# Kernel optimization log

Hardware: AMD Instinct MI355X
Metric: run time of the kernel (lower is better)

## Reference

```python
import jax, jax.numpy as jnp
import numpy as np

VOCAB, EMB, H, OUT = 32000, 512, 1024, 32000
SEQ, B = 512, 64

def setup_inputs() -> dict:
    key = jax.random.key(0)
    ks = jax.random.split(key, 16)
    sc = lambda *s: 1.0 / np.sqrt(s[-1])
    return {
        "x": jax.random.randint(ks[0], (B,), 0, VOCAB),
        "encoder_states": jax.random.normal(ks[1], (SEQ, B, 2 * H), jnp.float32),
        "hidden": jax.random.normal(ks[2], (1, B, H), jnp.float32),
        "cell": jax.random.normal(ks[3], (1, B, H), jnp.float32),
        "emb_table": jax.random.normal(ks[4], (VOCAB, EMB), jnp.float32),
        "energy_W": jax.random.normal(ks[5], (1, 3 * H), jnp.float32) * sc(1, 3 * H),
        "energy_b": jnp.zeros((1,), jnp.float32),
        "W_ih": jax.random.normal(ks[6], (4 * H, 2 * H + EMB), jnp.float32) * sc(1, H),
        "W_hh": jax.random.normal(ks[7], (4 * H, H), jnp.float32) * sc(1, H),
        "b_ih": jnp.zeros((4 * H,), jnp.float32),
        "b_hh": jnp.zeros((4 * H,), jnp.float32),
        "fc_W": jax.random.normal(ks[8], (OUT, H), jnp.float32) * sc(1, H),
        "fc_b": jnp.zeros((OUT,), jnp.float32),
    }

def reference(x, encoder_states, hidden, cell, emb_table, energy_W, energy_b,
              W_ih, W_hh, b_ih, b_hh, fc_W, fc_b):
    S = encoder_states.shape[0]
    emb = emb_table[x]                                     # [B, E] (dropout is identity at p=0)
    h_rep = jnp.broadcast_to(hidden, (S,) + hidden.shape[1:])   # [S, B, H]
    cat = jnp.concatenate([h_rep, encoder_states], axis=2)      # [S, B, 3H]
    energy = jax.nn.relu(jnp.einsum('sbk,ok->sbo', cat, energy_W) + energy_b)  # [S, B, 1]
    attn = jax.nn.softmax(energy[..., 0], axis=0)                # softmax over seq dim -> [S, B]
    context = jnp.einsum('sb,sbd->bd', attn, encoder_states)     # [B, 2H]
    rnn_in = jnp.concatenate([context, emb], axis=1)             # [B, 2H+E]
    gates = rnn_in @ W_ih.T + b_ih + hidden[0] @ W_hh.T + b_hh   # [B, 4H]
    i, f, g, o = jnp.split(gates, 4, axis=1)
    i, f, o = jax.nn.sigmoid(i), jax.nn.sigmoid(f), jax.nn.sigmoid(o)
    g = jnp.tanh(g)
    c_new = f * cell[0] + i * g
    h_new = o * jnp.tanh(c_new)
    preds = h_new @ fc_W.T + fc_b                                # [B, OUT]
    return preds, h_new[None], c_new[None]
```

## Files before the change

### kernel.cpp

```cpp
#include <hip/hip_runtime.h>

#define S_LEN 512
#define BATCH 64
#define HDIM  1024
#define TWOH  2048
#define EMB   512
#define KDIM  2560
#define KTOT  3584
#define VOUT  32000

#define WS_MS    64
#define WS_CTX   2112
#define WS_GP    WS_CTX
#define WS_RNNB  (WS_CTX + 64*16*2048)
#define WS_HB16  (WS_RNNB + 114688)

typedef __attribute__((ext_vector_type(8))) short bf16x8;
typedef __attribute__((ext_vector_type(4))) float f32x4;

__device__ __forceinline__ float sigmoidf_(float x) { return 1.f/(1.f+__expf(-x)); }

__device__ __forceinline__ unsigned short f2bf(float f) {
  union { float f; unsigned u; } v; v.f = f;
  return (unsigned short)((v.u + 0x7fffu + ((v.u >> 16) & 1u)) >> 16);
}

__global__ __launch_bounds__(256) void k_attn(const float* __restrict__ enc,
                                              const float* __restrict__ eW,
                                              const float* __restrict__ eb,
                                              const float* __restrict__ hidden,
                                              float* __restrict__ ws_ms,
                                              float* __restrict__ ws_ctx) {
  __shared__ float lds_ms[4][2];
  __shared__ float lds_ctx[4][2048];
  const int lane  = threadIdx.x & 63;
  const int wave  = threadIdx.x >> 6;
  const int chunk = blockIdx.x;
  const int b     = blockIdx.y;

  float hba = 0.f;
  for (int k = lane; k < HDIM; k += 64) hba += hidden[b*HDIM + k] * eW[k];
#pragma unroll
  for (int st = 32; st >= 1; st >>= 1) hba += __shfl_xor(hba, st, 64);
  const float hb = hba + eb[0];

  float4 w4[8];
#pragma unroll
  for (int k = 0; k < 8; ++k)
    w4[k] = *reinterpret_cast<const float4*>(eW + HDIM + 4*lane + 256*k);

  const int s0 = chunk*32 + wave*8;
  const float* base = enc + ((size_t)(s0*BATCH + b))*TWOH + 4*lane;

  float m = 0.f, ssum = 0.f;
  float4 ctx[8];
#pragma unroll
  for (int k = 0; k < 8; ++k) ctx[k] = make_float4(0.f, 0.f, 0.f, 0.f);

  float4 va[8], vb[8];
#pragma unroll
  for (int k = 0; k < 8; ++k) va[k] = *reinterpret_cast<const float4*>(base + 256*k);

#define ATTN_STEP(VCUR, VNXT, I)                                              \
  {                                                                           \
    if ((I) < 7) {                                                            \
      const float* pn = base + (size_t)((I)+1)*BATCH*TWOH;                    \
      _Pragma("unroll")                                                       \
      for (int k = 0; k < 8; ++k)                                             \
        VNXT[k] = *reinterpret_cast<const float4*>(pn + 256*k);               \
    }                                                                         \
    float a = 0.f;                                                            \
    _Pragma("unroll")                                                         \
    for (int k = 0; k < 8; ++k)                                               \
      a += VCUR[k].x*w4[k].x + VCUR[k].y*w4[k].y +                            \
           VCUR[k].z*w4[k].z + VCUR[k].w*w4[k].w;                             \
    _Pragma("unroll")                                                         \
    for (int st = 1; st < 64; st <<= 1) a += __shfl_xor(a, st, 64);           \
    const float e = fmaxf(a + hb, 0.f);                                       \
    if (e > m) {                                                              \
      const float sc = __expf(m - e);                                         \
      ssum = ssum*sc + 1.f;                                                   \
      _Pragma("unroll")                                                       \
      for (int k = 0; k < 8; ++k) {                                           \
        ctx[k].x = fmaf(ctx[k].x, sc, VCUR[k].x);                             \
        ctx[k].y = fmaf(ctx[k].y, sc, VCUR[k].y);                             \
        ctx[k].z = fmaf(ctx[k].z, sc, VCUR[k].z);                             \
        ctx[k].w = fmaf(ctx[k].w, sc, VCUR[k].w);                             \
      }                                                                       \
      m = e;                                                                  \
    } else {                                                                  \
      const float pw = __expf(e - m);                                         \
      ssum += pw;                                                             \
      _Pragma("unroll")                                                       \
      for (int k = 0; k < 8; ++k) {                                           \
        ctx[k].x = fmaf(pw, VCUR[k].x, ctx[k].x);                             \
        ctx[k].y = fmaf(pw, VCUR[k].y, ctx[k].y);                             \
        ctx[k].z = fmaf(pw, VCUR[k].z, ctx[k].z);                             \
        ctx[k].w = fmaf(pw, VCUR[k].w, ctx[k].w);                             \
      }                                                                       \
    }                                                                         \
  }

  ATTN_STEP(va, vb, 0)
  ATTN_STEP(vb, va, 1)
  ATTN_STEP(va, vb, 2)
  ATTN_STEP(vb, va, 3)
  ATTN_STEP(va, vb, 4)
  ATTN_STEP(vb, va, 5)
  ATTN_STEP(va, vb, 6)
  ATTN_STEP(vb, va, 7)
#undef ATTN_STEP

  if (lane == 0) { lds_ms[wave][0] = m; lds_ms[wave][1] = ssum; }
  __syncthreads();
  const float M = fmaxf(fmaxf(lds_ms[0][0], lds_ms[1][0]),
                        fmaxf(lds_ms[2][0], lds_ms[3][0]));
  const float wsc = __expf(m - M);
  float ssum_c = 0.f;
#pragma unroll
  for (int w = 0; w < 4; ++w) ssum_c += __expf(lds_ms[w][0] - M) * lds_ms[w][1];
#pragma unroll
  for (int k = 0; k < 8; ++k) {
    float4 c = ctx[k];
    c.x *= wsc; c.y *= wsc; c.z *= wsc; c.w *= wsc;
    *reinterpret_cast<float4*>(&lds_ctx[wave][4*lane + 256*k]) = c;
  }
  __syncthreads();
  float* outp = ws_ctx + ((size_t)b*16 + chunk)*TWOH;
  for (int d = threadIdx.x; d < TWOH; d += 256)
    outp[d] = lds_ctx[0][d] + lds_ctx[1][d] + lds_ctx[2][d] + lds_ctx[3][d];
  if (threadIdx.x == 0) {
    ws_ms[((size_t)b*16 + chunk)*2]     = M;
    ws_ms[((size_t)b*16 + chunk)*2 + 1] = ssum_c;
  }
}

__global__ __launch_bounds__(256) void k_combine(const float* __restrict__ ws_ms,
                                                 const float* __restrict__ ws_ctx,
                                                 const float* __restrict__ hidden,
                                                 const float* __restrict__ emb_table,
                                                 const int* __restrict__ x,
                                                 unsigned short* __restrict__ rnnB) {
  const int b = blockIdx.x;
  float mc[16], sc[16];
#pragma unroll
  for (int c = 0; c < 16; ++c) {
    mc[c] = ws_ms[(b*16 + c)*2];
    sc[c] = ws_ms[(b*16 + c)*2 + 1];
  }
  float M = mc[0];
#pragma unroll
  for (int c = 1; c < 16; ++c) M = fmaxf(M, mc[c]);
  float wc[16], Ssum = 0.f;
#pragma unroll
  for (int c = 0; c < 16; ++c) { wc[c] = __expf(mc[c] - M); Ssum += wc[c]*sc[c]; }
  const float inv = 1.f / Ssum;
  unsigned short* rb = rnnB + (size_t)b*KTOT;
  for (int d = threadIdx.x; d < TWOH; d += 256) {
    float a = 0.f;
#pragma unroll
    for (int c = 0; c < 16; ++c) a += wc[c] * ws_ctx[((size_t)b*16 + c)*TWOH + d];
    rb[d] = f2bf(a * inv);
  }
  const int xb = x[b];
  for (int e = threadIdx.x; e < EMB; e += 256)
    rb[TWOH + e] = f2bf(emb_table[(size_t)xb*EMB + e]);
  for (int k = threadIdx.x; k < HDIM; k += 256)
    rb[KDIM + k] = f2bf(hidden[b*HDIM + k]);
}

__global__ __launch_bounds__(256) void k_gates(const unsigned short* __restrict__ rnnB,
                                               const float* __restrict__ W_ih,
                                               const float* __restrict__ W_hh,
                                               float* __restrict__ ws_gp) {
  const int lane = threadIdx.x & 63;
  const int wave = threadIdx.x >> 6;
  const int part = blockIdx.x & 7;
  const int rg   = blockIdx.x >> 3;
  const int row0 = rg*64 + wave*16;
  const int mlo  = lane & 15;
  const int kg   = lane >> 4;
  const int j    = row0 + mlo;

  f32x4 acc0 = {0.f,0.f,0.f,0.f}, acc1 = acc0, acc2 = acc0, acc3 = acc0;

  for (int k0 = 0; k0 < 448; k0 += 32) {
    const int kbase = part*448 + k0;
    const float* wsrc = (kbase < KDIM)
        ? (W_ih + (size_t)j*KDIM + kbase + kg*8)
        : (W_hh + (size_t)j*HDIM + (kbase - KDIM) + kg*8);
    const float4 wa = *reinterpret_cast<const float4*>(wsrc);
    const float4 wb = *reinterpret_cast<const float4*>(wsrc + 4);
    bf16x8 afrag;
    afrag[0] = f2bf(wa.x); afrag[1] = f2bf(wa.y);
    afrag[2] = f2bf(wa.z); afrag[3] = f2bf(wa.w);
    afrag[4] = f2bf(wb.x); afrag[5] = f2bf(wb.y);
    afrag[6] = f2bf(wb.z); afrag[7] = f2bf(wb.w);

    const size_t ko = kbase + kg*8;
    const bf16x8 b0 = *reinterpret_cast<const bf16x8*>(rnnB + (size_t)(mlo     )*KTOT + ko);
    const bf16x8 b1 = *reinterpret_cast<const bf16x8*>(rnnB + (size_t)(mlo + 16)*KTOT + ko);
    const bf16x8 b2 = *reinterpret_cast<const bf16x8*>(rnnB + (size_t)(mlo + 32)*KTOT + ko);
    const bf16x8 b3 = *reinterpret_cast<const bf16x8*>(rnnB + (size_t)(mlo + 48)*KTOT + ko);

    acc0 = __builtin_amdgcn_mfma_f32_16x16x32_bf16(afrag, b0, acc0, 0, 0, 0);
    acc1 = __builtin_amdgcn_mfma_f32_16x16x32_bf16(afrag, b1, acc1, 0, 0, 0);
    acc2 = __builtin_amdgcn_mfma_f32_16x16x32_bf16(afrag, b2, acc2, 0, 0, 0);
    acc3 = __builtin_amdgcn_mfma_f32_16x16x32_bf16(afrag, b3, acc3, 0, 0, 0);
  }

  const int mbase = row0 + kg*4;
#define G_ST(ACC, N)                                                          \
  {                                                                           \
    _Pragma("unroll")                                                         \
    for (int jj = 0; jj < 4; ++jj)                                            \
      ws_gp[((size_t)part*4096 + mbase + jj)*64 + ((N)*16 + mlo)] = ACC[jj];  \
  }
  G_ST(acc0, 0) G_ST(acc1, 1) G_ST(acc2, 2) G_ST(acc3, 3)
#undef G_ST
}

__global__ __launch_bounds__(256) void k_lstm(const float* __restrict__ ws_gp,
                                              const float* __restrict__ b_ih,
                                              const float* __restrict__ b_hh,
                                              const float* __restrict__ cell,
                                              float* __restrict__ out_h,
                                              float* __restrict__ out_c,
                                              unsigned short* __restrict__ hB) {
  const int id = blockIdx.x*256 + threadIdx.x;
  const int h = id >> 6, b = id & 63;
  float g[4];
#pragma unroll
  for (int gg = 0; gg < 4; ++gg) {
    const int j = gg*1024 + h;
    float v = b_ih[j] + b_hh[j];
#pragma unroll
    for (int p = 0; p < 8; ++p) v += ws_gp[((size_t)p*4096 + j)*64 + b];
    g[gg] = v;
  }
  const float iv = sigmoidf_(g[0]);
  const float fv = sigmoidf_(g[1]);
  const float gv = tanhf(g[2]);
  const float ov = sigmoidf_(g[3]);
  const float cold = cell[b*HDIM + h];
  const float cn = fmaf(fv, cold, iv*gv);
  const float hn = ov * tanhf(cn);
  out_h[b*HDIM + h] = hn;
  out_c[b*HDIM + h] = cn;
  hB[(size_t)b*HDIM + h] = f2bf(hn);
}

__global__ __launch_bounds__(256) void k_fc(const unsigned short* __restrict__ hB,
                                            const float* __restrict__ fc_W,
                                            const float* __restrict__ fc_b,
                                            float* __restrict__ preds) {
  const int lane = threadIdx.x & 63;
  const int wave = threadIdx.x >> 6;
  const int row0 = (blockIdx.x*4 + wave)*16;
  const int mlo  = lane & 15;
  const int kg   = lane >> 4;

  const float* wrow = fc_W + (size_t)(row0 + mlo)*HDIM + kg*8;

  f32x4 acc0 = {0.f,0.f,0.f,0.f}, acc1 = acc0, acc2 = acc0, acc3 = acc0;

  for (int k0 = 0; k0 < HDIM; k0 += 32) {
    const float4 wa = *reinterpret_cast<const float4*>(wrow + k0);
    const float4 wb = *reinterpret_cast<const float4*>(wrow + k0 + 4);
    bf16x8 afrag;
    afrag[0] = f2bf(wa.x); afrag[1] = f2bf(wa.y);
    afrag[2] = f2bf(wa.z); afrag[3] = f2bf(wa.w);
    afrag[4] = f2bf(wb.x); afrag[5] = f2bf(wb.y);
    afrag[6] = f2bf(wb.z); afrag[7] = f2bf(wb.w);

    const size_t ko = k0 + kg*8;
    const bf16x8 b0 = *reinterpret_cast<const bf16x8*>(hB + (size_t)(mlo     )*HDIM + ko);
    const bf16x8 b1 = *reinterpret_cast<const bf16x8*>(hB + (size_t)(mlo + 16)*HDIM + ko);
    const bf16x8 b2 = *reinterpret_cast<const bf16x8*>(hB + (size_t)(mlo + 32)*HDIM + ko);
    const bf16x8 b3 = *reinterpret_cast<const bf16x8*>(hB + (size_t)(mlo + 48)*HDIM + ko);

    acc0 = __builtin_amdgcn_mfma_f32_16x16x32_bf16(afrag, b0, acc0, 0, 0, 0);
    acc1 = __builtin_amdgcn_mfma_f32_16x16x32_bf16(afrag, b1, acc1, 0, 0, 0);
    acc2 = __builtin_amdgcn_mfma_f32_16x16x32_bf16(afrag, b2, acc2, 0, 0, 0);
    acc3 = __builtin_amdgcn_mfma_f32_16x16x32_bf16(afrag, b3, acc3, 0, 0, 0);
  }

  const int mbase = row0 + kg*4;
  const float4 bias = make_float4(fc_b[mbase], fc_b[mbase+1],
                                  fc_b[mbase+2], fc_b[mbase+3]);
#define FC_STORE(ACC, N)                                                      \
  {                                                                           \
    float4 st = make_float4(ACC[0] + bias.x, ACC[1] + bias.y,                 \
                            ACC[2] + bias.z, ACC[3] + bias.w);                \
    *reinterpret_cast<float4*>(preds + (size_t)((N)*16 + mlo)*VOUT + mbase) = st; \
  }
  FC_STORE(acc0, 0) FC_STORE(acc1, 1) FC_STORE(acc2, 2) FC_STORE(acc3, 3)
#undef FC_STORE
}

extern "C" void kernel_launch(void* const* d_in, const int* in_sizes, int n_in,
                              void* d_out, int out_size, void* d_ws, size_t ws_size,
                              hipStream_t stream) {
  const int*   x      = (const int*)  d_in[0];
  const float* enc    = (const float*)d_in[1];
  const float* hidden = (const float*)d_in[2];
  const float* cell   = (const float*)d_in[3];
  const float* embt   = (const float*)d_in[4];
  const float* eW     = (const float*)d_in[5];
  const float* eb     = (const float*)d_in[6];
  const float* W_ih   = (const float*)d_in[7];
  const float* W_hh   = (const float*)d_in[8];
  const float* b_ih   = (const float*)d_in[9];
  const float* b_hh   = (const float*)d_in[10];
  const float* fc_W   = (const float*)d_in[11];
  const float* fc_b   = (const float*)d_in[12];

  float* out   = (float*)d_out;
  float* preds = out;
  float* out_h = out + (size_t)BATCH*VOUT;
  float* out_c = out_h + BATCH*HDIM;
  float* ws    = (float*)d_ws;
  unsigned short* rnnB = (unsigned short*)(ws + WS_RNNB);
  unsigned short* hB   = (unsigned short*)(ws + WS_HB16);

  k_attn<<<dim3(16, 64), 256, 0, stream>>>(enc, eW, eb, hidden, ws + WS_MS, ws + WS_CTX);
  k_combine<<<64, 256, 0, stream>>>(ws + WS_MS, ws + WS_CTX, hidden, embt, x, rnnB);
  k_gates<<<512, 256, 0, stream>>>(rnnB, W_ih, W_hh, ws + WS_GP);
  k_lstm<<<256, 256, 0, stream>>>(ws + WS_GP, b_ih, b_hh, cell, out_h, out_c, hB);
  k_fc<<<500, 256, 0, stream>>>(hB, fc_W, fc_b, preds);
}
```

Before: 150.5 us.

## Software-pipeline GEMV weight loads in gates/fc and widen combine grid

Both MFMA kernels (gates and fc) now fully unroll the K loop and double-buffer register fragments. The next 64-wide K slice of weights and activations is loaded while the current slice is converted to bf16 and fed to MFMA, which puts more memory requests in flight to hide global-load latency on the weight stream. The combine kernel now uses a 14x64 grid with one element per thread instead of 64 blocks looping. Register pressure rises from the doubled fragment buffers, and each combine thread recomputes the softmax chunk weights redundantly.

```diff
diff --git a/kernel.cpp b/kernel.cpp
--- a/kernel.cpp
+++ b/kernel.cpp
@@ -23,6 +23,15 @@
 __device__ __forceinline__ unsigned short f2bf(float f) {
   union { float f; unsigned u; } v; v.f = f;
   return (unsigned short)((v.u + 0x7fffu + ((v.u >> 16) & 1u)) >> 16);
+}
+
+__device__ __forceinline__ bf16x8 cvt_frag(const float4& a, const float4& b) {
+  bf16x8 r;
+  r[0] = (short)f2bf(a.x); r[1] = (short)f2bf(a.y);
+  r[2] = (short)f2bf(a.z); r[3] = (short)f2bf(a.w);
+  r[4] = (short)f2bf(b.x); r[5] = (short)f2bf(b.y);
+  r[6] = (short)f2bf(b.z); r[7] = (short)f2bf(b.w);
+  return r;
 }
 
 __global__ __launch_bounds__(256) void k_attn(const float* __restrict__ enc,
@@ -141,32 +150,34 @@
                                                  const float* __restrict__ emb_table,
                                                  const int* __restrict__ x,
                                                  unsigned short* __restrict__ rnnB) {
-  const int b = blockIdx.x;
-  float mc[16], sc[16];
-#pragma unroll
-  for (int c = 0; c < 16; ++c) {
-    mc[c] = ws_ms[(b*16 + c)*2];
-    sc[c] = ws_ms[(b*16 + c)*2 + 1];
-  }
-  float M = mc[0];
-#pragma unroll
-  for (int c = 1; c < 16; ++c) M = fmaxf(M, mc[c]);
-  float wc[16], Ssum = 0.f;
-#pragma unroll
-  for (int c = 0; c < 16; ++c) { wc[c] = __expf(mc[c] - M); Ssum += wc[c]*sc[c]; }
-  const float inv = 1.f / Ssum;
+  const int b = blockIdx.y;
+  const int k = blockIdx.x*256 + threadIdx.x;
   unsigned short* rb = rnnB + (size_t)b*KTOT;
-  for (int d = threadIdx.x; d < TWOH; d += 256) {
+
+  if (k < TWOH) {
+    float mc[16], sc[16];
+#pragma unroll
+    for (int c = 0; c < 16; ++c) {
+      mc[c] = ws_ms[(b*16 + c)*2];
+      sc[c] = ws_ms[(b*16 + c)*2 + 1];
+    }
+    float M = mc[0];
+#pragma unroll
+    for (int c = 1; c < 16; ++c) M = fmaxf(M, mc[c]);
+    float wc[16], Ssum = 0.f;
+#pragma unroll
+    for (int c = 0; c < 16; ++c) { wc[c] = __expf(mc[c] - M); Ssum += wc[c]*sc[c]; }
+    const float inv = 1.f / Ssum;
     float a = 0.f;
 #pragma unroll
-    for (int c = 0; c < 16; ++c) a += wc[c] * ws_ctx[((size_t)b*16 + c)*TWOH + d];
-    rb[d] = f2bf(a * inv);
-  }
-  const int xb = x[b];
-  for (int e = threadIdx.x; e < EMB; e += 256)
-    rb[TWOH + e] = f2bf(emb_table[(size_t)xb*EMB + e]);
-  for (int k = threadIdx.x; k < HDIM; k += 256)
-    rb[KDIM + k] = f2bf(hidden[b*HDIM + k]);
+    for (int c = 0; c < 16; ++c) a += wc[c] * ws_ctx[((size_t)b*16 + c)*TWOH + k];
+    rb[k] = f2bf(a * inv);
+  } else if (k < KDIM) {
+    const int xb = x[b];
+    rb[k] = f2bf(emb_table[(size_t)xb*EMB + (k - TWOH)]);
+  } else {
+    rb[k] = f2bf(hidden[b*HDIM + (k - KDIM)]);
+  }
 }
 
 __global__ __launch_bounds__(256) void k_gates(const unsigned short* __restrict__ rnnB,
@@ -181,33 +192,61 @@
   const int mlo  = lane & 15;
   const int kg   = lane >> 4;
   const int j    = row0 + mlo;
+  const unsigned short* rp0 = rnnB + (size_t)mlo*KTOT;
 
   f32x4 acc0 = {0.f,0.f,0.f,0.f}, acc1 = acc0, acc2 = acc0, acc3 = acc0;
 
-  for (int k0 = 0; k0 < 448; k0 += 32) {
-    const int kbase = part*448 + k0;
-    const float* wsrc = (kbase < KDIM)
-        ? (W_ih + (size_t)j*KDIM + kbase + kg*8)
-        : (W_hh + (size_t)j*HDIM + (kbase - KDIM) + kg*8);
-    const float4 wa = *reinterpret_cast<const float4*>(wsrc);
-    const float4 wb = *reinterpret_cast<const float4*>(wsrc + 4);
-    bf16x8 afrag;
-    afrag[0] = f2bf(wa.x); afrag[1] = f2bf(wa.y);
-    afrag[2] = f2bf(wa.z); afrag[3] = f2bf(wa.w);
-    afrag[4] = f2bf(wb.x); afrag[5] = f2bf(wb.y);
-    afrag[6] = f2bf(wb.z); afrag[7] = f2bf(wb.w);
-
-    const size_t ko = kbase + kg*8;
-    const bf16x8 b0 = *reinterpret_cast<const bf16x8*>(rnnB + (size_t)(mlo     )*KTOT + ko);
-    const bf16x8 b1 = *reinterpret_cast<const bf16x8*>(rnnB + (size_t)(mlo + 16)*KTOT + ko);
-    const bf16x8 b2 = *reinterpret_cast<const bf16x8*>(rnnB + (size_t)(mlo + 32)*KTOT + ko);
-    const bf16x8 b3 = *reinterpret_cast<const bf16x8*>(rnnB + (size_t)(mlo + 48)*KTOT + ko);
-
-    acc0 = __builtin_amdgcn_mfma_f32_16x16x32_bf16(afrag, b0, acc0, 0, 0, 0);
-    acc1 = __builtin_amdgcn_mfma_f32_16x16x32_bf16(afrag, b1, acc1, 0, 0, 0);
-    acc2 = __builtin_amdgcn_mfma_f32_16x16x32_bf16(afrag, b2, acc2, 0, 0, 0);
-    acc3 = __builtin_amdgcn_mfma_f32_16x16x32_bf16(afrag, b3, acc3, 0, 0, 0);
-  }
+  float4  Aa[4], Ab[4];
+  bf16x8  Ba[8], Bb[8];
+
+#define G_LOAD(AW, BB, S)                                                     \
+  {                                                                           \
+    const int kb0 = part*448 + (S)*64;                                        \
+    const int kb1 = kb0 + 32;                                                 \
+    const float* ws0 = (kb0 < KDIM) ? (W_ih + (size_t)j*KDIM + kb0 + kg*8)    \
+                                    : (W_hh + (size_t)j*HDIM + (kb0-KDIM) + kg*8); \
+    const float* ws1 = (kb1 < KDIM) ? (W_ih + (size_t)j*KDIM + kb1 + kg*8)    \
+                                    : (W_hh + (size_t)j*HDIM + (kb1-KDIM) + kg*8); \
+    AW[0] = *reinterpret_cast<const float4*>(ws0);                            \
+    AW[1] = *reinterpret_cast<const float4*>(ws0 + 4);                        \
+    AW[2] = *reinterpret_cast<const float4*>(ws1);                            \
+    AW[3] = *reinterpret_cast<const float4*>(ws1 + 4);                        \
+    const size_t ko0 = (size_t)kb0 + kg*8;                                    \
+    const size_t ko1 = (size_t)kb1 + kg*8;                                    \
+    BB[0] = *reinterpret_cast<const bf16x8*>(rp0 + ko0);                      \
+    BB[1] = *reinterpret_cast<const bf16x8*>(rp0 + 16*KTOT + ko0);            \
+    BB[2] = *reinterpret_cast<const bf16x8*>(rp0 + 32*KTOT + ko0);            \
+    BB[3] = *reinterpret_cast<const bf16x8*>(rp0 + 48*KTOT + ko0);            \
+    BB[4] = *reinterpret_cast<const bf16x8*>(rp0 + ko1);                      \
+    BB[5] = *reinterpret_cast<const bf16x8*>(rp0 + 16*KTOT + ko1);            \
+    BB[6] = *reinterpret_cast<const bf16x8*>(rp0 + 32*KTOT + ko1);            \
+    BB[7] = *reinterpret_cast<const bf16x8*>(rp0 + 48*KTOT + ko1);            \
+  }
+
+#define G_COMP(AW, BB)                                                        \
+  {                                                                           \
+    const bf16x8 af0 = cvt_frag(AW[0], AW[1]);                                \
+    const bf16x8 af1 = cvt_frag(AW[2], AW[3]);                                \
+    acc0 = __builtin_amdgcn_mfma_f32_16x16x32_bf16(af0, BB[0], acc0, 0, 0, 0);\
+    acc1 = __builtin_amdgcn_mfma_f32_16x16x32_bf16(af0, BB[1], acc1, 0, 0, 0);\
+    acc2 = __builtin_amdgcn_mfma_f32_16x16x32_bf16(af0, BB[2], acc2, 0, 0, 0);\
+    acc3 = __builtin_amdgcn_mfma_f32_16x16x32_bf16(af0, BB[3], acc3, 0, 0, 0);\
+    acc0 = __builtin_amdgcn_mfma_f32_16x16x32_bf16(af1, BB[4], acc0, 0, 0, 0);\
+    acc1 = __builtin_amdgcn_mfma_f32_16x16x32_bf16(af1, BB[5], acc1, 0, 0, 0);\
+    acc2 = __builtin_amdgcn_mfma_f32_16x16x32_bf16(af1, BB[6], acc2, 0, 0, 0);\
+    acc3 = __builtin_amdgcn_mfma_f32_16x16x32_bf16(af1, BB[7], acc3, 0, 0, 0);\
+  }
+
+  G_LOAD(Aa, Ba, 0)
+  G_LOAD(Ab, Bb, 1) G_COMP(Aa, Ba)
+  G_LOAD(Aa, Ba, 2) G_COMP(Ab, Bb)
+  G_LOAD(Ab, Bb, 3) G_COMP(Aa, Ba)
+  G_LOAD(Aa, Ba, 4) G_COMP(Ab, Bb)
+  G_LOAD(Ab, Bb, 5) G_COMP(Aa, Ba)
+  G_LOAD(Aa, Ba, 6) G_COMP(Ab, Bb)
+  G_COMP(Aa, Ba)
+#undef G_LOAD
+#undef G_COMP
 
   const int mbase = row0 + kg*4;
 #define G_ST(ACC, N)                                                          \
@@ -261,29 +300,62 @@
   const int kg   = lane >> 4;
 
   const float* wrow = fc_W + (size_t)(row0 + mlo)*HDIM + kg*8;
+  const unsigned short* hp = hB + (size_t)mlo*HDIM + kg*8;
 
   f32x4 acc0 = {0.f,0.f,0.f,0.f}, acc1 = acc0, acc2 = acc0, acc3 = acc0;
 
-  for (int k0 = 0; k0 < HDIM; k0 += 32) {
-    const float4 wa = *reinterpret_cast<const float4*>(wrow + k0);
-    const float4 wb = *reinterpret_cast<const float4*>(wrow + k0 + 4);
-    bf16x8 afrag;
-    afrag[0] = f2bf(wa.x); afrag[1] = f2bf(wa.y);
-    afrag[2] = f2bf(wa.z); afrag[3] = f2bf(wa.w);
-    afrag[4] = f2bf(wb.x); afrag[5] = f2bf(wb.y);
-    afrag[6] = f2bf(wb.z); afrag[7] = f2bf(wb.w);
-
-    const size_t ko = k0 + kg*8;
-    const bf16x8 b0 = *reinterpret_cast<const bf16x8*>(hB + (size_t)(mlo     )*HDIM + ko);
-    const bf16x8 b1 = *reinterpret_cast<const bf16x8*>(hB + (size_t)(mlo + 16)*HDIM + ko);
-    const bf16x8 b2 = *reinterpret_cast<const bf16x8*>(hB + (size_t)(mlo + 32)*HDIM + ko);
-    const bf16x8 b3 = *reinterpret_cast<const bf16x8*>(hB + (size_t)(mlo + 48)*HDIM + ko);
-
-    acc0 = __builtin_amdgcn_mfma_f32_16x16x32_bf16(afrag, b0, acc0, 0, 0, 0);
-    acc1 = __builtin_amdgcn_mfma_f32_16x16x32_bf16(afrag, b1, acc1, 0, 0, 0);
-    acc2 = __builtin_amdgcn_mfma_f32_16x16x32_bf16(afrag, b2, acc2, 0, 0, 0);
-    acc3 = __builtin_amdgcn_mfma_f32_16x16x32_bf16(afrag, b3, acc3, 0, 0, 0);
-  }
+  float4  Aa[4], Ab[4];
+  bf16x8  Ba[8], Bb[8];
+
+#define FC_LOAD(AW, BB, K0)                                                   \
+  {                                                                           \
+    AW[0] = *reinterpret_cast<const float4*>(wrow + (K0));                    \
+    AW[1] = *reinterpret_cast<const float4*>(wrow + (K0) + 4);                \
+    AW[2] = *reinterpret_cast<const float4*>(wrow + (K0) + 32);               \
+    AW[3] = *reinterpret_cast<const float4*>(wrow + (K0) + 36);               \
+    BB[0] = *reinterpret_cast<const bf16x8*>(hp + (K0));                      \
+    BB[1] = *reinterpret_cast<const bf16x8*>(hp + 16*HDIM + (K0));            \
+    BB[2] = *reinterpret_cast<const bf16x8*>(hp + 32*HDIM + (K0));            \
+    BB[3] = *reinterpret_cast<const bf16x8*>(hp + 48*HDIM + (K0));            \
+    BB[4] = *reinterpret_cast<const bf16x8*>(hp + (K0) + 32);                 \
+    BB[5] = *reinterpret_cast<const bf16x8*>(hp + 16*HDIM + (K0) + 32);       \
+    BB[6] = *reinterpret_cast<const bf16x8*>(hp + 32*HDIM + (K0) + 32);       \
+    BB[7] = *reinterpret_cast<const bf16x8*>(hp + 48*HDIM + (K0) + 32);       \
+  }
+
+#define FC_COMP(AW, BB)                                                       \
+  {                                                                           \
+    const bf16x8 af0 = cvt_frag(AW[0], AW[1]);                                \
+    const bf16x8 af1 = cvt_frag(AW[2], AW[3]);                                \
+    acc0 = __builtin_amdgcn_mfma_f32_16x16x32_bf16(af0, BB[0], acc0, 0, 0, 0);\
+    acc1 = __builtin_amdgcn_mfma_f32_16x16x32_bf16(af0, BB[1], acc1, 0, 0, 0);\
+    acc2 = __builtin_amdgcn_mfma_f32_16x16x32_bf16(af0, BB[2], acc2, 0, 0, 0);\
+    acc3 = __builtin_amdgcn_mfma_f32_16x16x32_bf16(af0, BB[3], acc3, 0, 0, 0);\
+    acc0 = __builtin_amdgcn_mfma_f32_16x16x32_bf16(af1, BB[4], acc0, 0, 0, 0);\
+    acc1 = __builtin_amdgcn_mfma_f32_16x16x32_bf16(af1, BB[5], acc1, 0, 0, 0);\
+    acc2 = __builtin_amdgcn_mfma_f32_16x16x32_bf16(af1, BB[6], acc2, 0, 0, 0);\
+    acc3 = __builtin_amdgcn_mfma_f32_16x16x32_bf16(af1, BB[7], acc3, 0, 0, 0);\
+  }
+
+  FC_LOAD(Aa, Ba, 0)
+  FC_LOAD(Ab, Bb, 64)  FC_COMP(Aa, Ba)
+  FC_LOAD(Aa, Ba, 128) FC_COMP(Ab, Bb)
+  FC_LOAD(Ab, Bb, 192) FC_COMP(Aa, Ba)
+  FC_LOAD(Aa, Ba, 256) FC_COMP(Ab, Bb)
+  FC_LOAD(Ab, Bb, 320) FC_COMP(Aa, Ba)
+  FC_LOAD(Aa, Ba, 384) FC_COMP(Ab, Bb)
+  FC_LOAD(Ab, Bb, 448) FC_COMP(Aa, Ba)
+  FC_LOAD(Aa, Ba, 512) FC_COMP(Ab, Bb)
+  FC_LOAD(Ab, Bb, 576) FC_COMP(Aa, Ba)
+  FC_LOAD(Aa, Ba, 640) FC_COMP(Ab, Bb)
+  FC_LOAD(Ab, Bb, 704) FC_COMP(Aa, Ba)
+  FC_LOAD(Aa, Ba, 768) FC_COMP(Ab, Bb)
+  FC_LOAD(Ab, Bb, 832) FC_COMP(Aa, Ba)
+  FC_LOAD(Aa, Ba, 896) FC_COMP(Ab, Bb)
+  FC_LOAD(Ab, Bb, 960) FC_COMP(Aa, Ba)
+  FC_COMP(Ab, Bb)
+#undef FC_LOAD
+#undef FC_COMP
 
   const int mbase = row0 + kg*4;
   const float4 bias = make_float4(fc_b[mbase], fc_b[mbase+1],
@@ -324,7 +396,7 @@
   unsigned short* hB   = (unsigned short*)(ws + WS_HB16);
 
   k_attn<<<dim3(16, 64), 256, 0, stream>>>(enc, eW, eb, hidden, ws + WS_MS, ws + WS_CTX);
-  k_combine<<<64, 256, 0, stream>>>(ws + WS_MS, ws + WS_CTX, hidden, embt, x, rnnB);
+  k_combine<<<dim3(14, 64), 256, 0, stream>>>(ws + WS_MS, ws + WS_CTX, hidden, embt, x, rnnB);
   k_gates<<<512, 256, 0, stream>>>(rnnB, W_ih, W_hh, ws + WS_GP);
   k_lstm<<<256, 256, 0, stream>>>(ws + WS_GP, b_ih, b_hh, cell, out_h, out_c, hB);
   k_fc<<<500, 256, 0, stream>>>(hB, fc_W, fc_b, preds);
```

Measured after the change: 145.9 us. -3.0%, faster.
